# Performance work log

Hardware: AMD Instinct MI355X
Metric: run time of the kernel (lower is better)

The kernel has to match this reference:

```python
import jax, jax.numpy as jnp
import numpy as np

N = 50000   # nodes
E = 600000  # edges
D = 128     # node_input_dim
H = 128     # hidden_dim
A = 200000  # number of valid actions


def setup_inputs() -> dict:
    key = jax.random.key(0)
    ks = jax.random.split(key, 8)
    x = jax.random.normal(ks[0], (N, D), dtype=jnp.float32)
    edge_index = jax.random.randint(ks[1], (2, E), 0, N, dtype=jnp.int64)
    valid_actions = jax.random.randint(ks[2], (A, 2), 0, N, dtype=jnp.int64)
    # GCNConv uses glorot-style init for weight, zeros/uniform for bias; exact init is irrelevant for correctness
    s1 = 1.0 / np.sqrt(D)
    sH = 1.0 / np.sqrt(H)
    s2 = 1.0 / np.sqrt(2 * H)
    W1 = jax.random.uniform(ks[3], (D, H), jnp.float32, -s1, s1)
    b1 = jax.random.uniform(ks[4], (H,), jnp.float32, -s1, s1)
    W2 = jax.random.uniform(ks[5], (H, H), jnp.float32, -sH, sH)
    b2 = jax.random.uniform(ks[6], (H,), jnp.float32, -sH, sH)
    Wq = jax.random.uniform(ks[7], (2 * H, 1), jnp.float32, -s2, s2)
    bq = jnp.zeros((1,), jnp.float32)
    return {"x": x, "edge_index": edge_index, "valid_actions": valid_actions,
            "W1": W1, "b1": b1, "W2": W2, "b2": b2, "Wq": Wq, "bq": bq}


def _gcn_conv(h, src, dst, norm, W, b, n_nodes):
    # PyG GCNConv: x' = D^{-1/2} (A + I) D^{-1/2} X W + b
    h = h @ W                              # [N, H]
    msg = h[src] * norm[:, None]           # [E+N, H] gather + scale
    out = jax.ops.segment_sum(msg, dst, num_segments=n_nodes)  # scatter-add
    return out + b


def reference(x, edge_index, valid_actions, W1, b1, W2, b2, Wq, bq):
    n = x.shape[0]
    loops = jnp.arange(n, dtype=edge_index.dtype)
    src = jnp.concatenate([edge_index[0], loops])  # self-loops appended
    dst = jnp.concatenate([edge_index[1], loops])
    # symmetric normalization from in-degree of A+I (unit edge weights)
    deg = jax.ops.segment_sum(jnp.ones_like(dst, x.dtype), dst, num_segments=n)
    dis = jnp.where(deg > 0, jax.lax.rsqrt(deg), 0.0)
    norm = dis[src] * dis[dst]             # [E+N]

    h = jax.nn.relu(_gcn_conv(x, src, dst, norm, W1, b1, n))
    h = jax.nn.relu(_gcn_conv(h, src, dst, norm, W2, b2, n))

    # batched gather-concat-linear replacing the per-action Python loop
    pair = jnp.concatenate([h[valid_actions[:, 0]], h[valid_actions[:, 1]]], axis=-1)  # [A, 2H]
    q = pair @ Wq + bq                     # [A, 1]
    return q.reshape(-1)                   # torch.cat of A scalars -> [A]
```

## Files before the change

kernel.cpp:

```cpp
#include <hip/hip_runtime.h>
#include <hip/hip_bf16.h>

#define HDIM 128

typedef __attribute__((ext_vector_type(8))) short bf16x8_t;
typedef __attribute__((ext_vector_type(4))) float f32x4_t;

__device__ inline float bf16u_to_f(unsigned int u) { return __uint_as_float(u << 16); }
__device__ inline unsigned short bf16_rne(float x) {
    union { __hip_bfloat16 b; unsigned short u; } cv;
    cv.b = __float2bfloat16(x);
    return cv.u;
}
__device__ inline void split2(float x, unsigned short& h, unsigned short& l) {
    h = bf16_rne(x);
    l = bf16_rne(x - __uint_as_float((unsigned int)h << 16));
}

__global__ void deg_count_k(const int* __restrict__ dst, int* __restrict__ deg, int E) {
    int i = blockIdx.x * blockDim.x + threadIdx.x;
    if (i < E) atomicAdd(&deg[dst[i]], 1);
}

__global__ void scan_part_k(const int* __restrict__ deg, int* __restrict__ incl,
                            int* __restrict__ blocksum, int N) {
    __shared__ int s[256];
    const int tid = threadIdx.x;
    const int i = blockIdx.x * 256 + tid;
    int v = (i < N) ? deg[i] : 0;
    s[tid] = v;
    __syncthreads();
    #pragma unroll
    for (int off = 1; off < 256; off <<= 1) {
        int t = (tid >= off) ? s[tid - off] : 0;
        __syncthreads();
        s[tid] += t;
        __syncthreads();
    }
    if (i < N) incl[i] = s[tid];
    if (tid == 255) blocksum[blockIdx.x] = s[255];
}

__global__ void scan_block_k(int* __restrict__ blocksum, int NB) {
    __shared__ int s[256];
    const int tid = threadIdx.x;
    int v = (tid < NB) ? blocksum[tid] : 0;
    s[tid] = v;
    __syncthreads();
    #pragma unroll
    for (int off = 1; off < 256; off <<= 1) {
        int t = (tid >= off) ? s[tid - off] : 0;
        __syncthreads();
        s[tid] += t;
        __syncthreads();
    }
    if (tid < NB) blocksum[tid] = s[tid] - v;
}

__global__ void scan_final_k(const int* __restrict__ deg, const int* __restrict__ incl,
                             const int* __restrict__ blocksum, int* __restrict__ rowptr,
                             float* __restrict__ dis, int N, int E) {
    const int i = blockIdx.x * 256 + threadIdx.x;
    if (i < N) {
        rowptr[i] = blocksum[blockIdx.x] + incl[i] - deg[i];
        dis[i] = rsqrtf((float)deg[i] + 1.0f);
    }
    if (i == 0) rowptr[N] = E;
}

__global__ void fill_csr_k(const int* __restrict__ src, const int* __restrict__ dst,
                           const int* __restrict__ rowptr, int* __restrict__ cursor,
                           int* __restrict__ csr, int E) {
    int e = blockIdx.x * blockDim.x + threadIdx.x;
    if (e < E) {
        const int d = dst[e];
        const int pos = rowptr[d] + atomicAdd(&cursor[d], 1);
        csr[pos] = src[e];
    }
}

__global__ void pack_w_k(const float* __restrict__ W, unsigned short* __restrict__ hi,
                         unsigned short* __restrict__ lo) {
    const int idx = blockIdx.x * 256 + threadIdx.x;
    const int frag = idx >> 9;
    const int r = idx & 511;
    const int lane = r >> 3, j = r & 7;
    const int c = frag & 7, s = frag >> 3;
    const int col = (c << 4) | (lane & 15);
    const int k = (s << 5) + ((lane >> 4) << 3) + j;
    const float w = W[k * HDIM + col];
    unsigned short h, l;
    split2(w, h, l);
    hi[idx] = h;
    lo[idx] = l;
}

__global__ void prep_x_k(const float* __restrict__ X, unsigned short* __restrict__ hi,
                         unsigned short* __restrict__ lo, int total4) {
    int i = blockIdx.x * blockDim.x + threadIdx.x;
    if (i >= total4) return;
    const float4 v = reinterpret_cast<const float4*>(X)[i];
    ushort4 h, l;
    split2(v.x, h.x, l.x);
    split2(v.y, h.y, l.y);
    split2(v.z, h.z, l.z);
    split2(v.w, h.w, l.w);
    reinterpret_cast<ushort4*>(hi)[i] = h;
    reinterpret_cast<ushort4*>(lo)[i] = l;
}

__global__ __launch_bounds__(256) void mfma_gemm_k(
    const unsigned short* __restrict__ Xh, const unsigned short* __restrict__ Xl,
    const unsigned short* __restrict__ Wp, const float* __restrict__ dis,
    float* __restrict__ hs, int N) {
    __shared__ __align__(16) unsigned short wlds[32768];
    const int tid = threadIdx.x;
    {
        const float4* wsrc = reinterpret_cast<const float4*>(Wp);
        float4* wdst = reinterpret_cast<float4*>(wlds);
        #pragma unroll
        for (int i = 0; i < 16; ++i) wdst[tid + i * 256] = wsrc[tid + i * 256];
    }
    __syncthreads();

    const int wave = tid >> 6, lane = tid & 63;
    const int row0 = (blockIdx.x << 6) + (wave << 4);
    if (row0 >= N) return;
    const int lrow = lane & 15;
    const int kgrp = (lane >> 4) << 3;

    const long abase = ((long)(row0 + lrow) << 7) + kgrp;
    bf16x8_t ah[4], al[4];
    #pragma unroll
    for (int s = 0; s < 4; ++s) {
        ah[s] = *reinterpret_cast<const bf16x8_t*>(Xh + abase + (s << 5));
        al[s] = *reinterpret_cast<const bf16x8_t*>(Xl + abase + (s << 5));
    }

    f32x4_t acc[8];
    #pragma unroll
    for (int c = 0; c < 8; ++c) acc[c] = (f32x4_t){0.f, 0.f, 0.f, 0.f};

    #pragma unroll
    for (int s = 0; s < 4; ++s) {
        #pragma unroll
        for (int c = 0; c < 8; ++c) {
            const int fo = (((s << 3) + c) << 9) + (lane << 3);
            const bf16x8_t bh = *reinterpret_cast<const bf16x8_t*>(wlds + fo);
            const bf16x8_t bl = *reinterpret_cast<const bf16x8_t*>(wlds + 16384 + fo);
            acc[c] = __builtin_amdgcn_mfma_f32_16x16x32_bf16(ah[s], bh, acc[c], 0, 0, 0);
            acc[c] = __builtin_amdgcn_mfma_f32_16x16x32_bf16(al[s], bh, acc[c], 0, 0, 0);
            acc[c] = __builtin_amdgcn_mfma_f32_16x16x32_bf16(ah[s], bl, acc[c], 0, 0, 0);
        }
    }

    const int rbase = row0 + ((lane >> 4) << 2);
    float d[4];
    #pragma unroll
    for (int i = 0; i < 4; ++i) d[i] = dis[rbase + i];
    #pragma unroll
    for (int c = 0; c < 8; ++c) {
        const int col = (c << 4) | lrow;
        #pragma unroll
        for (int i = 0; i < 4; ++i)
            hs[((long)(rbase + i) << 7) + col] = acc[c][i] * d[i];
    }
}

__global__ __launch_bounds__(256) void gather_agg_k(
    const int* __restrict__ rowptr, const int* __restrict__ csr,
    const float* __restrict__ hs, const float* __restrict__ dis,
    const float* __restrict__ b, unsigned short* __restrict__ oh,
    unsigned short* __restrict__ ol, int N) {
    const int lane = threadIdx.x & 63;
    const int wid = (int)((blockIdx.x * (long)blockDim.x + threadIdx.x) >> 6);
    const int nw = (int)(((long)gridDim.x * blockDim.x) >> 6);
    const float2 bb = *reinterpret_cast<const float2*>(&b[lane * 2]);
    for (int n = wid; n < N; n += nw) {
        const int r0 = rowptr[n], r1 = rowptr[n + 1];
        float2 acc = *reinterpret_cast<const float2*>(&hs[((long)n << 7) + lane * 2]);
        int e = r0;
        for (; e + 2 <= r1; e += 2) {
            const int s0 = csr[e], s1 = csr[e + 1];
            const float2 v0 = *reinterpret_cast<const float2*>(&hs[((long)s0 << 7) + lane * 2]);
            const float2 v1 = *reinterpret_cast<const float2*>(&hs[((long)s1 << 7) + lane * 2]);
            acc.x += v0.x + v1.x;
            acc.y += v0.y + v1.y;
        }
        if (e < r1) {
            const int s0 = csr[e];
            const float2 v0 = *reinterpret_cast<const float2*>(&hs[((long)s0 << 7) + lane * 2]);
            acc.x += v0.x;
            acc.y += v0.y;
        }
        const float dv = dis[n];
        const float o0 = fmaxf(fmaf(acc.x, dv, bb.x), 0.f);
        const float o1 = fmaxf(fmaf(acc.y, dv, bb.y), 0.f);
        ushort2 h, l;
        split2(o0, h.x, l.x);
        split2(o1, h.y, l.y);
        *reinterpret_cast<ushort2*>(oh + ((long)n << 7) + lane * 2) = h;
        *reinterpret_cast<ushort2*>(ol + ((long)n << 7) + lane * 2) = l;
    }
}

__global__ __launch_bounds__(256) void qhead_k(
    const unsigned short* __restrict__ hh, const unsigned short* __restrict__ hl,
    const int* __restrict__ va, const float* __restrict__ Wq,
    const float* __restrict__ bq, float* __restrict__ out, int A) {
    const int lane = threadIdx.x & 63;
    int w = (int)((blockIdx.x * (long)blockDim.x + threadIdx.x) >> 6);
    const int nw = (int)(((long)gridDim.x * blockDim.x) >> 6);
    const float2 wu = *reinterpret_cast<const float2*>(&Wq[lane * 2]);
    const float2 wv = *reinterpret_cast<const float2*>(&Wq[HDIM + lane * 2]);
    const float bqv = bq[0];
    for (int a = w; a < A; a += nw) {
        const int u = va[2 * a], v = va[2 * a + 1];
        unsigned int ph = *reinterpret_cast<const unsigned int*>(hh + ((long)u << 7) + (lane << 1));
        unsigned int pl = *reinterpret_cast<const unsigned int*>(hl + ((long)u << 7) + (lane << 1));
        const float u0 = bf16u_to_f(ph) + bf16u_to_f(pl);
        const float u1 = __uint_as_float(ph & 0xffff0000u) + __uint_as_float(pl & 0xffff0000u);
        ph = *reinterpret_cast<const unsigned int*>(hh + ((long)v << 7) + (lane << 1));
        pl = *reinterpret_cast<const unsigned int*>(hl + ((long)v << 7) + (lane << 1));
        const float v0 = bf16u_to_f(ph) + bf16u_to_f(pl);
        const float v1 = __uint_as_float(ph & 0xffff0000u) + __uint_as_float(pl & 0xffff0000u);
        float s = u0 * wu.x + u1 * wu.y + v0 * wv.x + v1 * wv.y;
        #pragma unroll
        for (int off = 32; off > 0; off >>= 1) s += __shfl_down(s, off, 64);
        if (lane == 0) out[a] = s + bqv;
    }
}

extern "C" void kernel_launch(void* const* d_in, const int* in_sizes, int n_in,
                              void* d_out, int out_size, void* d_ws, size_t ws_size,
                              hipStream_t stream) {
    const float* x   = (const float*)d_in[0];
    const int*   ei  = (const int*)d_in[1];
    const int*   va  = (const int*)d_in[2];
    const float* W1  = (const float*)d_in[3];
    const float* b1  = (const float*)d_in[4];
    const float* W2  = (const float*)d_in[5];
    const float* b2  = (const float*)d_in[6];
    const float* Wq  = (const float*)d_in[7];
    const float* bq  = (const float*)d_in[8];
    float* out = (float*)d_out;

    const int N = in_sizes[0] / HDIM;
    const int E = in_sizes[1] / 2;
    const int A = in_sizes[2] / 2;
    const int* esrc = ei;
    const int* edst = ei + E;

    char* p = (char*)d_ws;
    auto alloc = [&](size_t bytes) { char* r = p; p += (bytes + 255) & ~(size_t)255; return r; };
    int* deg_i    = (int*)alloc((size_t)N * 4);
    int* incl     = (int*)alloc((size_t)N * 4);
    int* rowptr   = (int*)alloc((size_t)(N + 1) * 4);
    int* cursor   = (int*)alloc((size_t)N * 4);
    int* blocksum = (int*)alloc(256 * 4);
    int* csr      = (int*)alloc((size_t)E * 4);
    float* dis    = (float*)alloc((size_t)N * 4);
    unsigned short* Wp1 = (unsigned short*)alloc(32768 * 2);
    unsigned short* Wp2 = (unsigned short*)alloc(32768 * 2);
    unsigned short* Xh  = (unsigned short*)alloc((size_t)N * HDIM * 2);
    unsigned short* Xl  = (unsigned short*)alloc((size_t)N * HDIM * 2);
    float* bufA   = (float*)alloc((size_t)N * HDIM * 4);

    const int T = 256;
    const int NB = (N + 255) / 256;

    hipMemsetAsync(deg_i, 0, (size_t)N * 4, stream);
    hipMemsetAsync(cursor, 0, (size_t)N * 4, stream);
    deg_count_k<<<(E + T - 1) / T, T, 0, stream>>>(edst, deg_i, E);
    scan_part_k<<<NB, 256, 0, stream>>>(deg_i, incl, blocksum, N);
    scan_block_k<<<1, 256, 0, stream>>>(blocksum, NB);
    scan_final_k<<<NB, 256, 0, stream>>>(deg_i, incl, blocksum, rowptr, dis, N, E);
    fill_csr_k<<<(E + T - 1) / T, T, 0, stream>>>(esrc, edst, rowptr, cursor, csr, E);

    pack_w_k<<<64, 256, 0, stream>>>(W1, Wp1, Wp1 + 16384);
    pack_w_k<<<64, 256, 0, stream>>>(W2, Wp2, Wp2 + 16384);
    prep_x_k<<<(N * HDIM / 4 + T - 1) / T, T, 0, stream>>>(x, Xh, Xl, N * HDIM / 4);

    mfma_gemm_k<<<(N + 63) / 64, 256, 0, stream>>>(Xh, Xl, Wp1, dis, bufA, N);
    gather_agg_k<<<2048, T, 0, stream>>>(rowptr, csr, bufA, dis, b1, Xh, Xl, N);

    mfma_gemm_k<<<(N + 63) / 64, 256, 0, stream>>>(Xh, Xl, Wp2, dis, bufA, N);
    gather_agg_k<<<2048, T, 0, stream>>>(rowptr, csr, bufA, dis, b2, Xh, Xl, N);

    qhead_k<<<4096, T, 0, stream>>>(Xh, Xl, va, Wq, bq, out, A);
}
```

Baseline: 321.4 us.

## Precompute per-node Q-head projections and unroll gather aggregation by four

The Q head is linear over the concatenated pair, so each node's hidden vector is now projected onto the two halves of Wq once (N dot products) instead of gathering two 128-wide rows per action. The per-action kernel becomes one thread per action doing two scalar lookups and an add, which replaces about A*2*512 bytes of row gathers with small scalar gathers. Separately, the gather-aggregation loop is unrolled to four neighbours with two accumulators to expose more memory-level parallelism. The cost is one extra kernel launch and a slightly different floating-point summation order.

```diff
diff --git a/kernel.cpp b/kernel.cpp
--- a/kernel.cpp
+++ b/kernel.cpp
@@ -176,58 +176,79 @@
     const int wid = (int)((blockIdx.x * (long)blockDim.x + threadIdx.x) >> 6);
     const int nw = (int)(((long)gridDim.x * blockDim.x) >> 6);
     const float2 bb = *reinterpret_cast<const float2*>(&b[lane * 2]);
+    const int loff = lane * 2;
     for (int n = wid; n < N; n += nw) {
         const int r0 = rowptr[n], r1 = rowptr[n + 1];
-        float2 acc = *reinterpret_cast<const float2*>(&hs[((long)n << 7) + lane * 2]);
+        float2 acc = *reinterpret_cast<const float2*>(&hs[((long)n << 7) + loff]);
+        float2 acc2 = {0.f, 0.f};
         int e = r0;
-        for (; e + 2 <= r1; e += 2) {
-            const int s0 = csr[e], s1 = csr[e + 1];
-            const float2 v0 = *reinterpret_cast<const float2*>(&hs[((long)s0 << 7) + lane * 2]);
-            const float2 v1 = *reinterpret_cast<const float2*>(&hs[((long)s1 << 7) + lane * 2]);
+        for (; e + 4 <= r1; e += 4) {
+            const int s0 = csr[e], s1 = csr[e + 1], s2 = csr[e + 2], s3 = csr[e + 3];
+            const float2 v0 = *reinterpret_cast<const float2*>(&hs[((long)s0 << 7) + loff]);
+            const float2 v1 = *reinterpret_cast<const float2*>(&hs[((long)s1 << 7) + loff]);
+            const float2 v2 = *reinterpret_cast<const float2*>(&hs[((long)s2 << 7) + loff]);
+            const float2 v3 = *reinterpret_cast<const float2*>(&hs[((long)s3 << 7) + loff]);
             acc.x += v0.x + v1.x;
             acc.y += v0.y + v1.y;
-        }
-        if (e < r1) {
+            acc2.x += v2.x + v3.x;
+            acc2.y += v2.y + v3.y;
+        }
+        for (; e < r1; ++e) {
             const int s0 = csr[e];
-            const float2 v0 = *reinterpret_cast<const float2*>(&hs[((long)s0 << 7) + lane * 2]);
+            const float2 v0 = *reinterpret_cast<const float2*>(&hs[((long)s0 << 7) + loff]);
             acc.x += v0.x;
             acc.y += v0.y;
         }
+        acc.x += acc2.x;
+        acc.y += acc2.y;
         const float dv = dis[n];
         const float o0 = fmaxf(fmaf(acc.x, dv, bb.x), 0.f);
         const float o1 = fmaxf(fmaf(acc.y, dv, bb.y), 0.f);
         ushort2 h, l;
         split2(o0, h.x, l.x);
         split2(o1, h.y, l.y);
-        *reinterpret_cast<ushort2*>(oh + ((long)n << 7) + lane * 2) = h;
-        *reinterpret_cast<ushort2*>(ol + ((long)n << 7) + lane * 2) = l;
-    }
-}
-
-__global__ __launch_bounds__(256) void qhead_k(
+        *reinterpret_cast<ushort2*>(oh + ((long)n << 7) + loff) = h;
+        *reinterpret_cast<ushort2*>(ol + ((long)n << 7) + loff) = l;
+    }
+}
+
+__global__ __launch_bounds__(256) void proj_k(
     const unsigned short* __restrict__ hh, const unsigned short* __restrict__ hl,
-    const int* __restrict__ va, const float* __restrict__ Wq,
-    const float* __restrict__ bq, float* __restrict__ out, int A) {
+    const float* __restrict__ Wq, float* __restrict__ pu, float* __restrict__ pv, int N) {
     const int lane = threadIdx.x & 63;
-    int w = (int)((blockIdx.x * (long)blockDim.x + threadIdx.x) >> 6);
+    const int wid = (int)((blockIdx.x * (long)blockDim.x + threadIdx.x) >> 6);
     const int nw = (int)(((long)gridDim.x * blockDim.x) >> 6);
     const float2 wu = *reinterpret_cast<const float2*>(&Wq[lane * 2]);
     const float2 wv = *reinterpret_cast<const float2*>(&Wq[HDIM + lane * 2]);
+    for (int n = wid; n < N; n += nw) {
+        const unsigned int ph = *reinterpret_cast<const unsigned int*>(hh + ((long)n << 7) + (lane << 1));
+        const unsigned int pl = *reinterpret_cast<const unsigned int*>(hl + ((long)n << 7) + (lane << 1));
+        const float h0 = bf16u_to_f(ph) + bf16u_to_f(pl);
+        const float h1 = __uint_as_float(ph & 0xffff0000u) + __uint_as_float(pl & 0xffff0000u);
+        float su = h0 * wu.x + h1 * wu.y;
+        float sv = h0 * wv.x + h1 * wv.y;
+        #pragma unroll
+        for (int off = 32; off > 0; off >>= 1) {
+            su += __shfl_down(su, off, 64);
+            sv += __shfl_down(sv, off, 64);
+        }
+        if (lane == 0) {
+            pu[n] = su;
+            pv[n] = sv;
+        }
+    }
+}
+
+__global__ __launch_bounds__(256) void qhead_k(
+    const float* __restrict__ pu, const float* __restrict__ pv,
+    const int* __restrict__ va, const float* __restrict__ bq,
+    float* __restrict__ out, int A) {
     const float bqv = bq[0];
-    for (int a = w; a < A; a += nw) {
-        const int u = va[2 * a], v = va[2 * a + 1];
-        unsigned int ph = *reinterpret_cast<const unsigned int*>(hh + ((long)u << 7) + (lane << 1));
-        unsigned int pl = *reinterpret_cast<const unsigned int*>(hl + ((long)u << 7) + (lane << 1));
-        const float u0 = bf16u_to_f(ph) + bf16u_to_f(pl);
-        const float u1 = __uint_as_float(ph & 0xffff0000u) + __uint_as_float(pl & 0xffff0000u);
-        ph = *reinterpret_cast<const unsigned int*>(hh + ((long)v << 7) + (lane << 1));
-        pl = *reinterpret_cast<const unsigned int*>(hl + ((long)v << 7) + (lane << 1));
-        const float v0 = bf16u_to_f(ph) + bf16u_to_f(pl);
-        const float v1 = __uint_as_float(ph & 0xffff0000u) + __uint_as_float(pl & 0xffff0000u);
-        float s = u0 * wu.x + u1 * wu.y + v0 * wv.x + v1 * wv.y;
-        #pragma unroll
-        for (int off = 32; off > 0; off >>= 1) s += __shfl_down(s, off, 64);
-        if (lane == 0) out[a] = s + bqv;
+    int i = blockIdx.x * blockDim.x + threadIdx.x;
+    const int stride = gridDim.x * blockDim.x;
+    for (; i < A; i += stride) {
+        const int2 uv = reinterpret_cast<const int2*>(va)[i];
+        out[i] = pu[uv.x] + pv[uv.y] + bqv;
     }
 }
 
@@ -260,6 +281,8 @@
     int* blocksum = (int*)alloc(256 * 4);
     int* csr      = (int*)alloc((size_t)E * 4);
     float* dis    = (float*)alloc((size_t)N * 4);
+    float* pu     = (float*)alloc((size_t)N * 4);
+    float* pv     = (float*)alloc((size_t)N * 4);
     unsigned short* Wp1 = (unsigned short*)alloc(32768 * 2);
     unsigned short* Wp2 = (unsigned short*)alloc(32768 * 2);
     unsigned short* Xh  = (unsigned short*)alloc((size_t)N * HDIM * 2);
@@ -287,5 +310,6 @@
     mfma_gemm_k<<<(N + 63) / 64, 256, 0, stream>>>(Xh, Xl, Wp2, dis, bufA, N);
     gather_agg_k<<<2048, T, 0, stream>>>(rowptr, csr, bufA, dis, b2, Xh, Xl, N);
 
-    qhead_k<<<4096, T, 0, stream>>>(Xh, Xl, va, Wq, bq, out, A);
-}
+    proj_k<<<2048, T, 0, stream>>>(Xh, Xl, Wq, pu, pv, N);
+    qhead_k<<<512, T, 0, stream>>>(pu, pv, va, bq, out, A);
+}
```

Result: faster. 297.1 us (-7.6%).
